# Optimization experiments

Measured on AMD Instinct MI355X. Metric: run time of the kernel, lower is better.

The kernel has to match this reference:

```python
import jax, jax.numpy as jnp
import numpy as np

D_MODEL = 1024
HEADS = 16
D_K = D_MODEL // HEADS
B, S = 2, 2048
NEG = -1e9


def setup_inputs() -> dict:
    key = jax.random.key(0)
    ks = jax.random.split(key, 12)
    sc = 1.0 / np.sqrt(D_MODEL)
    inp = {
        'query': jax.random.normal(ks[0], (B, S, D_MODEL), jnp.float32),
        'key': jax.random.normal(ks[1], (B, S, D_MODEL), jnp.float32),
        'value': jax.random.normal(ks[2], (B, S, D_MODEL), jnp.float32),
        'mask': jnp.tril(jnp.ones((S, S), jnp.int32))[None, None],  # [1,1,S,S] causal
        'Wq': jax.random.normal(ks[3], (D_MODEL, D_MODEL), jnp.float32) * sc,
        'bq': jax.random.normal(ks[4], (D_MODEL,), jnp.float32) * 0.02,
        'Wk': jax.random.normal(ks[5], (D_MODEL, D_MODEL), jnp.float32) * sc,
        'bk': jax.random.normal(ks[6], (D_MODEL,), jnp.float32) * 0.02,
        'Wv': jax.random.normal(ks[7], (D_MODEL, D_MODEL), jnp.float32) * sc,
        'bv': jax.random.normal(ks[8], (D_MODEL,), jnp.float32) * 0.02,
        'Wo': jax.random.normal(ks[9], (D_MODEL, D_MODEL), jnp.float32) * sc,
        'bo': jax.random.normal(ks[10], (D_MODEL,), jnp.float32) * 0.02,
    }
    return inp


def reference(query, key, value, mask, Wq, bq, Wk, bk, Wv, bv, Wo, bo):
    # QKV projections (torch Linear: x @ W.T + b; here W stored as [in,out])
    def split_heads(x):  # [B,S,D] -> [B,H,S,dk]
        return x.reshape(B, S, HEADS, D_K).transpose(0, 2, 1, 3)

    q = split_heads(query @ Wq + bq)
    k = split_heads(key @ Wk + bk)
    v = split_heads(value @ Wv + bv)

    scores = jnp.einsum('bhqd,bhkd->bhqk', q, k) / np.sqrt(D_K)
    scores = jnp.where(mask == 0, NEG, scores)
    attn = jax.nn.softmax(scores, axis=-1)  # dropout p=0 (eval) -> identity
    out = jnp.einsum('bhqk,bhkd->bhqd', attn, v)
    out = out.transpose(0, 2, 1, 3).reshape(B, S, D_MODEL)
    return out @ Wo + bo
```

## Files before the change

kernel.cpp:

```cpp
#include <hip/hip_runtime.h>
#include <hip/hip_bf16.h>
#include <cstdint>
#include <cstddef>

typedef short short8 __attribute__((ext_vector_type(8)));
typedef float f32x4 __attribute__((ext_vector_type(4)));
typedef float f32x16 __attribute__((ext_vector_type(16)));

#define SS 2048
#define DK 64
#define LAMBDA 0.18033688011112042f

#define CH 528

__device__ __forceinline__ float b2f(ushort u) {
    union { uint32_t i; float f; } x; x.i = ((uint32_t)u) << 16; return x.f;
}
__device__ __forceinline__ ushort f2b(float f) {
    union { float f; uint32_t i; } x; x.f = f;
    uint32_t r = (x.i + 0x7fffu + ((x.i >> 16) & 1u)) >> 16;
    return (ushort)r;
}
__device__ __forceinline__ uint32_t pk_bf16(float a, float b) {
    union { __hip_bfloat162 v; uint32_t u; } x;
    float2 f2; f2.x = a; f2.y = b;
    x.v = __float22bfloat162_rn(f2);
    return x.u;
}

__device__ __forceinline__ void gl_lds16(const ushort* __restrict__ g, ushort* l) {
    __builtin_amdgcn_global_load_lds(
        (const __attribute__((address_space(1))) uint32_t*)(uintptr_t)g,
        (__attribute__((address_space(3))) uint32_t*)(uintptr_t)l, 16, 0, 0);
}

__device__ __forceinline__ bool probe_bf16(const uint32_t* __restrict__ probe) {
    const int lane = threadIdx.x & 63;
    int c = 0;
#pragma unroll
    for (int i = 0; i < 4; ++i) {
        uint32_t u = probe[lane * 4 + i];
        uint32_t e = (u >> 7) & 0xffu;
        c += (e >= 100u && e <= 140u) ? 1 : 0;
    }
    unsigned long long b = __ballot(c >= 3);
    return __popcll(b) > 32;
}

__device__ __forceinline__ void ld8_f32_to_bf16(ushort* dst, const float* __restrict__ src) {
    float4 a = *(const float4*)src;
    float4 b = *(const float4*)(src + 4);
    ushort t[8] = {f2b(a.x), f2b(a.y), f2b(a.z), f2b(a.w),
                   f2b(b.x), f2b(b.y), f2b(b.z), f2b(b.w)};
    *(uint4*)dst = *(uint4*)t;
}

__global__ __launch_bounds__(256) void transpose_all(const void* __restrict__ W0,
                                                     const void* __restrict__ W1,
                                                     const void* __restrict__ W2,
                                                     const void* __restrict__ W3,
                                                     ushort* __restrict__ ws,
                                                     const uint32_t* __restrict__ probe,
                                                     size_t wotOff) {
    __shared__ __align__(16) ushort t[64 * 72];
    const bool isbf = probe_bf16(probe);
    const int z = blockIdx.z;
    const void* W = (z == 0) ? W0 : (z == 1) ? W1 : (z == 2) ? W2 : W3;
    ushort* T = ws + ((z < 3) ? ((size_t)z << 20) : wotOff);

    const int n0 = blockIdx.x * 64, k0 = blockIdx.y * 64;
    const int tid = threadIdx.x;
    const int r = tid >> 3, cg = (tid & 7) * 8;
    if (isbf) {
        const ushort* Wb = (const ushort*)W;
#pragma unroll
        for (int p = 0; p < 2; ++p) {
            int k = r + p * 32;
            *(uint4*)&t[k * 72 + cg] = *(const uint4*)&Wb[(size_t)(k0 + k) * 1024 + n0 + cg];
        }
    } else {
        const float* Wf = (const float*)W;
#pragma unroll
        for (int p = 0; p < 2; ++p) {
            int k = r + p * 32;
            ld8_f32_to_bf16(&t[k * 72 + cg], &Wf[(size_t)(k0 + k) * 1024 + n0 + cg]);
        }
    }
    __syncthreads();
#pragma unroll
    for (int p = 0; p < 2; ++p) {
        int n = r + p * 32;
        uint4 o;
        ushort* op = (ushort*)&o;
#pragma unroll
        for (int i = 0; i < 8; ++i) op[i] = t[(cg + i) * 72 + n];
        *(uint4*)&T[(size_t)(n0 + n) * 1024 + k0 + cg] = o;
    }
}

__global__ __launch_bounds__(256) void conv_qkv(const void* __restrict__ q,
                                                const void* __restrict__ k,
                                                const void* __restrict__ v,
                                                ushort* __restrict__ ws,
                                                const uint32_t* __restrict__ probe,
                                                size_t dstOff) {
    const bool isbf = probe_bf16(probe);
    if (isbf) return;
    const int z = blockIdx.y;
    const void* src = (z == 0) ? q : (z == 1) ? k : v;
    ushort* dst = ws + dstOff + ((size_t)z << 22);
    const size_t i = ((size_t)blockIdx.x * 256 + threadIdx.x) * 8;
    ld8_f32_to_bf16(&dst[i], &((const float*)src)[i]);
}

template <int PRE>
__global__ __launch_bounds__(256, 3) void qkv_gemm(const void* __restrict__ qp,
                                                   const void* __restrict__ kp,
                                                   const void* __restrict__ vp,
                                                   const void* __restrict__ bqp,
                                                   const void* __restrict__ bkp,
                                                   const void* __restrict__ bvp,
                                                   ushort* __restrict__ ws,
                                                   const uint32_t* __restrict__ probe) {
    __shared__ __align__(16) ushort As[3][128 * 32];
    __shared__ __align__(16) ushort Bs[3][128 * 32];
    const bool isbf = probe_bf16(probe);
    const int z = blockIdx.z;
    const ushort* Bt = ws + ((size_t)z << 20);
    const void* bias = (z == 0) ? bqp : (z == 1) ? bkp : bvp;
    ushort* C = ws + ((size_t)((PRE ? 16 : 5) + 4 * z) << 20);
    const float scl = (z == 0) ? LAMBDA : 1.0f;

    const int tid = threadIdx.x;
    const int lane = tid & 63, wid = tid >> 6;
    const int l15 = lane & 15, g = lane >> 4;
    const int wm = wid >> 1, wn = wid & 1;
    const int id0 = blockIdx.y * 8 + blockIdx.x;
    const int id = (id0 & 7) * 32 + (id0 >> 3);
    const int m0 = (id >> 3) * 128, n0 = (id & 7) * 128;
    const int sr = tid >> 2, sc = (tid & 3) * 8;
    const int lrow = (lane >> 2), lcol = (lane & 3) * 8;

    f32x4 acc[4][4];
#pragma unroll
    for (int i = 0; i < 4; ++i)
#pragma unroll
        for (int j = 0; j < 4; ++j) {
            f32x4 zz = {0.f, 0.f, 0.f, 0.f};
            acc[i][j] = zz;
        }

    if (PRE) {
        const ushort* Ab = isbf ? (const ushort*)((z == 0) ? qp : (z == 1) ? kp : vp)
                                : ws + ((size_t)(4 + 4 * z) << 20);
        auto stage1 = [&](int kk, int bsel) {
#pragma unroll
            for (int q = 0; q < 2; ++q) {
                const int row = (wid * 2 + q) * 16 + lrow;
                gl_lds16(&Bt[(size_t)(n0 + row) * 1024 + kk + lcol],
                         &Bs[bsel][(wid * 2 + q) * 512]);
                gl_lds16(&Ab[(size_t)(m0 + row) * 1024 + kk + lcol],
                         &As[bsel][(wid * 2 + q) * 512]);
            }
        };
        stage1(0, 0);
        stage1(32, 1);
        asm volatile("s_waitcnt vmcnt(4)" ::: "memory");
        __builtin_amdgcn_s_barrier();
        __builtin_amdgcn_sched_barrier(0);
        int cur = 0;
#pragma unroll 1
        for (int kk = 0; kk < 1024; kk += 32) {
            const int nxt = (cur >= 1) ? cur - 1 : cur + 2;
            if (kk + 64 < 1024) stage1(kk + 64, nxt);
            short8 a[4], b[4];
#pragma unroll
            for (int i = 0; i < 4; ++i)
                a[i] = *(const short8*)&As[cur][(wm * 64 + i * 16 + l15) * 32 + g * 8];
#pragma unroll
            for (int j = 0; j < 4; ++j)
                b[j] = *(const short8*)&Bs[cur][(wn * 64 + j * 16 + l15) * 32 + g * 8];
#pragma unroll
            for (int i = 0; i < 4; ++i)
#pragma unroll
                for (int j = 0; j < 4; ++j)
                    acc[i][j] =
                        __builtin_amdgcn_mfma_f32_16x16x32_bf16(a[i], b[j], acc[i][j], 0, 0, 0);
            if (kk + 32 < 1024) {
                if (kk + 64 < 1024)
                    asm volatile("s_waitcnt vmcnt(4)" ::: "memory");
                else
                    asm volatile("s_waitcnt vmcnt(0)" ::: "memory");
                __builtin_amdgcn_s_barrier();
                __builtin_amdgcn_sched_barrier(0);
            }
            cur = (cur == 2) ? 0 : cur + 1;
        }
    } else {
        auto stageAB = [&](int kk, int bsel) {
#pragma unroll
            for (int q = 0; q < 2; ++q) {
                const int row = (wid * 2 + q) * 16 + lrow;
                gl_lds16(&Bt[(size_t)(n0 + row) * 1024 + kk + lcol],
                         &Bs[bsel][(wid * 2 + q) * 512]);
            }
            const void* A = (z == 0) ? qp : (z == 1) ? kp : vp;
            if (isbf) {
                const ushort* Ab = (const ushort*)A;
#pragma unroll
                for (int q = 0; q < 2; ++q) {
                    const int row = (wid * 2 + q) * 16 + lrow;
                    gl_lds16(&Ab[(size_t)(m0 + row) * 1024 + kk + lcol],
                             &As[bsel][(wid * 2 + q) * 512]);
                }
            } else {
                const float* Af = (const float*)A;
                ld8_f32_to_bf16(&As[bsel][sr * 32 + sc], &Af[(size_t)(m0 + sr) * 1024 + kk + sc]);
                ld8_f32_to_bf16(&As[bsel][(sr + 64) * 32 + sc],
                                &Af[(size_t)(m0 + sr + 64) * 1024 + kk + sc]);
            }
        };
        stageAB(0, 0);
        __syncthreads();
#pragma unroll 2
        for (int kk = 0; kk < 1024; kk += 32) {
            const int cur = (kk >> 5) & 1;
            if (kk < 1024 - 32) stageAB(kk + 32, cur ^ 1);
            short8 a[4], b[4];
#pragma unroll
            for (int i = 0; i < 4; ++i)
                a[i] = *(const short8*)&As[cur][(wm * 64 + i * 16 + l15) * 32 + g * 8];
#pragma unroll
            for (int j = 0; j < 4; ++j)
                b[j] = *(const short8*)&Bs[cur][(wn * 64 + j * 16 + l15) * 32 + g * 8];
#pragma unroll
            for (int i = 0; i < 4; ++i)
#pragma unroll
                for (int j = 0; j < 4; ++j)
                    acc[i][j] =
                        __builtin_amdgcn_mfma_f32_16x16x32_bf16(a[i], b[j], acc[i][j], 0, 0, 0);
            __syncthreads();
        }
    }

#pragma unroll
    for (int i = 0; i < 4; ++i)
#pragma unroll
        for (int j = 0; j < 4; ++j) {
            const int col = n0 + wn * 64 + j * 16 + l15;
            const float bv = isbf ? b2f(((const ushort*)bias)[col]) : ((const float*)bias)[col];
#pragma unroll
            for (int r = 0; r < 4; ++r) {
                const int row = m0 + wm * 64 + i * 16 + g * 4 + r;
                const float v = (acc[i][j][r] + bv) * scl;
                size_t idx;
                if (z != 2) {
                    idx = ((size_t)((row >> 11) * 16 + (col >> 6)) * SS + (row & 2047)) * 64 +
                          (col & 63);
                } else {
                    idx = ((size_t)((row >> 11) * 16 + (col >> 6)) * 64 + (col & 63)) * SS +
                          (row & 2047);
                }
                C[idx] = f2b(v);
            }
        }
}

__global__ __launch_bounds__(256) void out_gemm(const ushort* __restrict__ A,
                                                const ushort* __restrict__ Bt,
                                                const void* __restrict__ bias,
                                                void* __restrict__ C,
                                                const uint32_t* __restrict__ probe) {
    __shared__ __align__(16) ushort As[3][64 * 32];
    __shared__ __align__(16) ushort Bs[3][128 * 32];
    const bool isbf = probe_bf16(probe);
    const int tid = threadIdx.x;
    const int lane = tid & 63, wid = tid >> 6;
    const int l15 = lane & 15, g = lane >> 4;
    const int wm = wid >> 1, wn = wid & 1;
    const int id0 = blockIdx.y * 8 + blockIdx.x;
    const int id = (id0 & 7) * 64 + (id0 >> 3);
    const int m0 = (id >> 3) * 64, n0 = (id & 7) * 128;
    const int lrow = (lane >> 2), lcol = (lane & 3) * 8;

    f32x4 acc[2][4];
#pragma unroll
    for (int i = 0; i < 2; ++i)
#pragma unroll
        for (int j = 0; j < 4; ++j) {
            f32x4 zz = {0.f, 0.f, 0.f, 0.f};
            acc[i][j] = zz;
        }

    auto stage1 = [&](int kk, int bsel) {
        {
            const int row = wid * 16 + lrow;
            gl_lds16(&A[(size_t)(m0 + row) * 1024 + kk + lcol], &As[bsel][wid * 512]);
        }
#pragma unroll
        for (int q = 0; q < 2; ++q) {
            const int row = (wid * 2 + q) * 16 + lrow;
            gl_lds16(&Bt[(size_t)(n0 + row) * 1024 + kk + lcol], &Bs[bsel][(wid * 2 + q) * 512]);
        }
    };

    stage1(0, 0);
    stage1(32, 1);
    asm volatile("s_waitcnt vmcnt(3)" ::: "memory");
    __builtin_amdgcn_s_barrier();
    __builtin_amdgcn_sched_barrier(0);
    int cur = 0;
#pragma unroll 1
    for (int kk = 0; kk < 1024; kk += 32) {
        const int nxt = (cur >= 1) ? cur - 1 : cur + 2;
        if (kk + 64 < 1024) stage1(kk + 64, nxt);
        short8 a[2], b[4];
#pragma unroll
        for (int i = 0; i < 2; ++i)
            a[i] = *(const short8*)&As[cur][(wm * 32 + i * 16 + l15) * 32 + g * 8];
#pragma unroll
        for (int j = 0; j < 4; ++j)
            b[j] = *(const short8*)&Bs[cur][(wn * 64 + j * 16 + l15) * 32 + g * 8];
#pragma unroll
        for (int i = 0; i < 2; ++i)
#pragma unroll
            for (int j = 0; j < 4; ++j)
                acc[i][j] = __builtin_amdgcn_mfma_f32_16x16x32_bf16(a[i], b[j], acc[i][j], 0, 0, 0);
        if (kk + 32 < 1024) {
            if (kk + 64 < 1024)
                asm volatile("s_waitcnt vmcnt(3)" ::: "memory");
            else
                asm volatile("s_waitcnt vmcnt(0)" ::: "memory");
            __builtin_amdgcn_s_barrier();
            __builtin_amdgcn_sched_barrier(0);
        }
        cur = (cur == 2) ? 0 : cur + 1;
    }

#pragma unroll
    for (int i = 0; i < 2; ++i)
#pragma unroll
        for (int j = 0; j < 4; ++j) {
            const int col = n0 + wn * 64 + j * 16 + l15;
            const float bv = isbf ? b2f(((const ushort*)bias)[col]) : ((const float*)bias)[col];
#pragma unroll
            for (int r = 0; r < 4; ++r) {
                const int row = m0 + wm * 32 + i * 16 + g * 4 + r;
                const float v = acc[i][j][r] + bv;
                const size_t idx = (size_t)row * 1024 + col;
                if (isbf)
                    ((ushort*)C)[idx] = f2b(v);
                else
                    ((float*)C)[idx] = v;
            }
        }
}

__global__ __launch_bounds__(256, 2) void attn_fwd(const ushort* __restrict__ Q,
                                                   const ushort* __restrict__ K,
                                                   const ushort* __restrict__ Vt,
                                                   ushort* __restrict__ O) {
    __shared__ __align__(16) ushort Ks[3][8 * CH];
    __shared__ __align__(16) ushort Vs[3][8 * CH];

    const int y = blockIdx.y;
    const int s0i = (blockIdx.x + y) & 15;
    const int t = (y & 16) ? (15 - s0i) : s0i;
    const int tid = threadIdx.x;
    const int lane = tid & 63, wid = tid >> 6;
    const int l31 = lane & 31, h = lane >> 5;

    const ushort* Qb = Q + (size_t)y * SS * DK;
    const ushort* Kb = K + (size_t)y * SS * DK;
    const ushort* Vb = Vt + (size_t)y * DK * SS;
    const int b = y >> 4, hh = y & 15;

    const int q0w = t * 128 + wid * 32;
    const int nkt = 2 * t + 2;

    const int srow = lane >> 3;
    const int sgc = ((lane & 7) ^ srow) * 8;

    short8 qf[4];
#pragma unroll
    for (int k4 = 0; k4 < 4; ++k4)
        qf[k4] = *(const short8*)&Qb[(size_t)(q0w + l31) * 64 + k4 * 16 + h * 8];

    int foff[2][4];
#pragma unroll
    for (int aa = 0; aa < 2; ++aa)
#pragma unroll
        for (int k4 = 0; k4 < 4; ++k4)
            foff[aa][k4] = (aa * 4 + (l31 >> 3)) * CH + (l31 & 7) * 64 +
                           (((k4 * 2 + h) ^ (l31 & 7)) * 8);

    f32x16 acc[2];
#pragma unroll
    for (int nt = 0; nt < 2; ++nt)
#pragma unroll
        for (int r = 0; r < 16; ++r) acc[nt][r] = 0.f;
    float lpA = 0.f, lpB = 0.f;

    auto stageKV = [&](int kt, int bsel) {
#pragma unroll
        for (int i = 0; i < 2; ++i) {
            const int chunk = wid * 2 + i;
            const int row = chunk * 8 + srow;
            gl_lds16(&Kb[(size_t)(kt * 64 + row) * 64 + sgc], &Ks[bsel][chunk * CH]);
            gl_lds16(&Vb[(size_t)row * SS + kt * 64 + sgc], &Vs[bsel][chunk * CH]);
        }
    };

    stageKV(0, 0);
    stageKV(1, 1);
    asm volatile("s_waitcnt vmcnt(4)" ::: "memory");
    __builtin_amdgcn_s_barrier();
    __builtin_amdgcn_sched_barrier(0);

    int cur = 0;
#pragma unroll 1
    for (int kt = 0; kt < nkt; ++kt) {
        if (kt + 2 < nkt) {
            const int nxt = (cur >= 1) ? cur - 1 : cur + 2;
            stageKV(kt + 2, nxt);
        }

        if (q0w + 31 >= kt * 64) {
            f32x16 sc[2];
#pragma unroll
            for (int st = 0; st < 2; ++st)
#pragma unroll
                for (int r = 0; r < 16; ++r) sc[st][r] = 0.f;
#pragma unroll
            for (int st = 0; st < 2; ++st)
#pragma unroll
                for (int k4 = 0; k4 < 4; ++k4) {
                    short8 kb = *(const short8*)&Ks[cur][foff[st][k4]];
                    sc[st] = __builtin_amdgcn_mfma_f32_32x32x16_bf16(kb, qf[k4], sc[st], 0, 0, 0);
                }

            if (kt >= nkt - 2) {
                const int qg = q0w + l31;
#pragma unroll
                for (int st = 0; st < 2; ++st)
#pragma unroll
                    for (int r = 0; r < 16; ++r) {
                        const int kvg = kt * 64 + st * 32 + (r & 3) + 8 * (r >> 2) + 4 * h;
                        if (kvg > qg) sc[st][r] = -1e9f;
                    }
            }

            uint32_t pk8[2][8];
#pragma unroll
            for (int st = 0; st < 2; ++st) {
                float ls = 0.f;
#pragma unroll
                for (int i = 0; i < 8; ++i) {
                    const float p0 = exp2f(sc[st][2 * i]);
                    const float p1 = exp2f(sc[st][2 * i + 1]);
                    ls += p0 + p1;
                    pk8[st][i] = pk_bf16(p0, p1);
                }
                if (st == 0) lpA += ls; else lpB += ls;
            }

#pragma unroll
            for (int st = 0; st < 2; ++st) {
                asm("v_permlane32_swap_b32 %0, %1" : "+v"(pk8[st][0]), "+v"(pk8[st][2]));
                asm("v_permlane32_swap_b32 %0, %1" : "+v"(pk8[st][1]), "+v"(pk8[st][3]));
                asm("v_permlane32_swap_b32 %0, %1" : "+v"(pk8[st][4]), "+v"(pk8[st][6]));
                asm("v_permlane32_swap_b32 %0, %1" : "+v"(pk8[st][5]), "+v"(pk8[st][7]));
            }

#pragma unroll
            for (int ktv = 0; ktv < 4; ++ktv) {
                union { uint32_t u[4]; short8 s; } pa;
#pragma unroll
                for (int w4 = 0; w4 < 4; ++w4) pa.u[w4] = pk8[ktv >> 1][(ktv & 1) * 4 + w4];
#pragma unroll
                for (int nt = 0; nt < 2; ++nt) {
                    short8 vb = *(const short8*)&Vs[cur][foff[nt][ktv]];
                    acc[nt] =
                        __builtin_amdgcn_mfma_f32_32x32x16_bf16(pa.s, vb, acc[nt], 0, 0, 0);
                }
            }
        }

        if (kt + 1 < nkt) {
            if (kt + 2 < nkt)
                asm volatile("s_waitcnt vmcnt(4)" ::: "memory");
            else
                asm volatile("s_waitcnt vmcnt(0)" ::: "memory");
            __builtin_amdgcn_s_barrier();
            __builtin_amdgcn_sched_barrier(0);
        }
        cur = (cur == 2) ? 0 : cur + 1;
    }

    const float lp = lpA + lpB;
    const float lt = lp + __shfl_xor(lp, 32);
    const float inv = 1.0f / lt;
#pragma unroll
    for (int r = 0; r < 16; ++r) {
        const int qrow = (r & 3) + 8 * (r >> 2) + 4 * h;
        const float ivr = __shfl(inv, qrow);
        const int rowg = q0w + qrow;
#pragma unroll
        for (int nt = 0; nt < 2; ++nt) {
            const int col = hh * 64 + nt * 32 + l31;
            O[(size_t)(b * SS + rowg) * 1024 + col] = f2b(acc[nt][r] * ivr);
        }
    }
}

extern "C" void kernel_launch(void* const* d_in, const int* in_sizes, int n_in,
                              void* d_out, int out_size, void* d_ws, size_t ws_size,
                              hipStream_t stream) {
    const void* q = d_in[0];
    const void* k = d_in[1];
    const void* v = d_in[2];
    const void* Wq = d_in[4];
    const void* bq = d_in[5];
    const void* Wk = d_in[6];
    const void* bk = d_in[7];
    const void* Wv = d_in[8];
    const void* bv = d_in[9];
    const void* Wo = d_in[10];
    const void* bo = d_in[11];
    const uint32_t* probe = (const uint32_t*)d_in[0];

    ushort* ws = (ushort*)d_ws;
    const size_t M = (size_t)1 << 20;
    const bool pre = ws_size >= 28 * M * sizeof(ushort);

    if (pre) {
        transpose_all<<<dim3(16, 16, 4), 256, 0, stream>>>(Wq, Wk, Wv, Wo, ws, probe, 3 * M);
        conv_qkv<<<dim3(2048, 3), 256, 0, stream>>>(q, k, v, ws, probe, 4 * M);
        qkv_gemm<1><<<dim3(8, 32, 3), 256, 0, stream>>>(q, k, v, bq, bk, bv, ws, probe);
        attn_fwd<<<dim3(16, 32), 256, 0, stream>>>(ws + 16 * M, ws + 20 * M, ws + 24 * M,
                                                   ws + 4 * M);
        out_gemm<<<dim3(8, 64), 256, 0, stream>>>(ws + 4 * M, ws + 3 * M, bo, d_out, probe);
    } else {
        transpose_all<<<dim3(16, 16, 4), 256, 0, stream>>>(Wq, Wk, Wv, Wo, ws, probe, 4 * M);
        qkv_gemm<0><<<dim3(8, 32, 3), 256, 0, stream>>>(q, k, v, bq, bk, bv, ws, probe);
        attn_fwd<<<dim3(16, 32), 256, 0, stream>>>(ws + 5 * M, ws + 9 * M, ws + 13 * M, ws);
        out_gemm<<<dim3(8, 64), 256, 0, stream>>>(ws, ws + 4 * M, bo, d_out, probe);
    }
}
```

Measured before the change: 234.4 us.

## Stage K/V tiles into LDS in MFMA fragment order for linear reads

Changes the global-to-LDS staging so each lane loads exactly the 16-byte fragment it will later feed to the MFMA. Each fragment is stored contiguously at (fragment*512 + lane*8). This replaces the padded, XOR-swizzled row layout (CH=528), so LDS reads become simple linear lane-strided accesses with no bank-conflict padding or per-lane offset table. The trade-off is less coalesced global loads: each lane now reads a 16-byte piece from a different row, whereas before eight lanes covered one contiguous 128-byte row segment.

Measured after the change: 234.7 us. Within noise of the previous version (+0.1%).

```diff
diff --git a/kernel.cpp b/kernel.cpp
--- a/kernel.cpp
+++ b/kernel.cpp
@@ -10,8 +10,6 @@
 #define SS 2048
 #define DK 64
 #define LAMBDA 0.18033688011112042f
-
-#define CH 528
 
 __device__ __forceinline__ float b2f(ushort u) {
     union { uint32_t i; float f; } x; x.i = ((uint32_t)u) << 16; return x.f;
@@ -360,8 +358,8 @@
                                                    const ushort* __restrict__ K,
                                                    const ushort* __restrict__ Vt,
                                                    ushort* __restrict__ O) {
-    __shared__ __align__(16) ushort Ks[3][8 * CH];
-    __shared__ __align__(16) ushort Vs[3][8 * CH];
+    __shared__ __align__(16) ushort Ks[3][8 * 512];
+    __shared__ __align__(16) ushort Vs[3][8 * 512];
 
     const int y = blockIdx.y;
     const int s0i = (blockIdx.x + y) & 15;
@@ -378,21 +376,18 @@
     const int q0w = t * 128 + wid * 32;
     const int nkt = 2 * t + 2;
 
-    const int srow = lane >> 3;
-    const int sgc = ((lane & 7) ^ srow) * 8;
-
     short8 qf[4];
 #pragma unroll
     for (int k4 = 0; k4 < 4; ++k4)
         qf[k4] = *(const short8*)&Qb[(size_t)(q0w + l31) * 64 + k4 * 16 + h * 8];
 
-    int foff[2][4];
-#pragma unroll
-    for (int aa = 0; aa < 2; ++aa)
-#pragma unroll
-        for (int k4 = 0; k4 < 4; ++k4)
-            foff[aa][k4] = (aa * 4 + (l31 >> 3)) * CH + (l31 & 7) * 64 +
-                           (((k4 * 2 + h) ^ (l31 & 7)) * 8);
+    const int f0 = wid * 2, f1 = f0 + 1;
+    const ushort* kb0 = Kb + (size_t)((f0 >> 2) * 32 + l31) * 64 + (f0 & 3) * 16 + h * 8;
+    const ushort* kb1 = Kb + (size_t)((f1 >> 2) * 32 + l31) * 64 + (f1 & 3) * 16 + h * 8;
+    const ushort* vb0 = Vb + (size_t)((f0 >> 2) * 32 + l31) * SS + (f0 & 3) * 16 + h * 8;
+    const ushort* vb1 = Vb + (size_t)((f1 >> 2) * 32 + l31) * SS + (f1 & 3) * 16 + h * 8;
+
+    const int lo8 = lane * 8;
 
     f32x16 acc[2];
 #pragma unroll
@@ -402,13 +397,12 @@
     float lpA = 0.f, lpB = 0.f;
 
     auto stageKV = [&](int kt, int bsel) {
-#pragma unroll
-        for (int i = 0; i < 2; ++i) {
-            const int chunk = wid * 2 + i;
-            const int row = chunk * 8 + srow;
-            gl_lds16(&Kb[(size_t)(kt * 64 + row) * 64 + sgc], &Ks[bsel][chunk * CH]);
-            gl_lds16(&Vb[(size_t)row * SS + kt * 64 + sgc], &Vs[bsel][chunk * CH]);
-        }
+        const size_t ko = (size_t)kt * 4096;
+        const int vo = kt * 64;
+        gl_lds16(kb0 + ko, &Ks[bsel][f0 * 512]);
+        gl_lds16(kb1 + ko, &Ks[bsel][f1 * 512]);
+        gl_lds16(vb0 + vo, &Vs[bsel][f0 * 512]);
+        gl_lds16(vb1 + vo, &Vs[bsel][f1 * 512]);
     };
 
     stageKV(0, 0);
@@ -435,7 +429,7 @@
             for (int st = 0; st < 2; ++st)
 #pragma unroll
                 for (int k4 = 0; k4 < 4; ++k4) {
-                    short8 kb = *(const short8*)&Ks[cur][foff[st][k4]];
+                    short8 kb = *(const short8*)&Ks[cur][(st * 4 + k4) * 512 + lo8];
                     sc[st] = __builtin_amdgcn_mfma_f32_32x32x16_bf16(kb, qf[k4], sc[st], 0, 0, 0);
                 }
 
@@ -479,7 +473,7 @@
                 for (int w4 = 0; w4 < 4; ++w4) pa.u[w4] = pk8[ktv >> 1][(ktv & 1) * 4 + w4];
 #pragma unroll
                 for (int nt = 0; nt < 2; ++nt) {
-                    short8 vb = *(const short8*)&Vs[cur][foff[nt][ktv]];
+                    short8 vb = *(const short8*)&Vs[cur][(nt * 4 + ktv) * 512 + lo8];
                     acc[nt] =
                         __builtin_amdgcn_mfma_f32_32x32x16_bf16(pa.s, vb, acc[nt], 0, 0, 0);
                 }
```
